# Optimization experiments

Measured on AMD Instinct MI355X. Metric: run time of the kernel, lower is better.

The kernel has to match this reference:

```python
import jax, jax.numpy as jnp
import numpy as np

N = 131072   # total nodes in batch
E = 524288   # directed edges
B = 2048     # number of graphs
H = 128      # hidden_dim
NF = 30      # node_feature_dim
GF = 4415    # gene_feature_dim
L = 3        # gnn_layers
EPS = 1e-5   # batchnorm eps


def setup_inputs() -> dict:
    key = jax.random.key(0)
    ks = jax.random.split(key, 24)
    rn = lambda k, s, sc=0.05: jax.random.normal(k, s, jnp.float32) * sc
    return {
        "x": jax.random.normal(ks[0], (N, NF), jnp.float32),
        "gene_features": jax.random.normal(ks[1], (B, GF), jnp.float32),
        "edge_index": jax.random.randint(ks[2], (2, E), 0, N),
        "batch": (jnp.arange(N) * B) // N,  # sorted, every graph non-empty
        "W_emb": rn(ks[3], (NF, H)), "b_emb": jnp.zeros((H,), jnp.float32),
        "Wg": rn(ks[4], (L, H, H)), "bg": jnp.zeros((L, H), jnp.float32),
        "bn_gamma": jnp.ones((L, H), jnp.float32), "bn_beta": jnp.zeros((L, H), jnp.float32),
        "Wd1": rn(ks[5], (2 * H, H)), "bd1": jnp.zeros((H,), jnp.float32),
        "Wd2": rn(ks[6], (H, H)), "bd2": jnp.zeros((H,), jnp.float32),
        "Wge1": rn(ks[7], (GF, 256)), "bge1": jnp.zeros((256,), jnp.float32),
        "g_gamma": jnp.ones((256,), jnp.float32), "g_beta": jnp.zeros((256,), jnp.float32),
        "Wge2": rn(ks[8], (256, H)), "bge2": jnp.zeros((H,), jnp.float32),
        "Wh1": rn(ks[9], (2 * H, H)), "bh1": jnp.zeros((H,), jnp.float32),
        "h_gamma": jnp.ones((H,), jnp.float32), "h_beta": jnp.zeros((H,), jnp.float32),
        "Wh2": rn(ks[10], (H, 64)), "bh2": jnp.zeros((64,), jnp.float32),
        "Wh3": rn(ks[11], (64, 1)), "bh3": jnp.zeros((1,), jnp.float32),
    }


def _bn_eval(x, gamma, beta):
    # inference batchnorm with running_mean=0, running_var=1
    return x * (gamma / jnp.sqrt(1.0 + EPS)) + beta


def _gcn_conv(h, W, b, src, dst):
    # PyG GCNConv: add self-loops, symmetric deg normalization, W first, bias after agg
    hw = h @ W                                            # [N,H]
    loop = jnp.arange(N)
    src_a = jnp.concatenate([src, loop])                  # [E+N]
    dst_a = jnp.concatenate([dst, loop])
    deg = jax.ops.segment_sum(jnp.ones((E + N,), hw.dtype), dst_a, num_segments=N)
    dinv = jnp.where(deg > 0, jax.lax.rsqrt(deg), 0.0)
    norm = dinv[src_a] * dinv[dst_a]                      # [E+N]
    msgs = hw[src_a] * norm[:, None]                      # gather [E+N,H]
    out = jax.ops.segment_sum(msgs, dst_a, num_segments=N)
    return out + b


def reference(x, gene_features, edge_index, batch, W_emb, b_emb, Wg, bg, bn_gamma,
              bn_beta, Wd1, bd1, Wd2, bd2, Wge1, bge1, g_gamma, g_beta, Wge2, bge2,
              Wh1, bh1, h_gamma, h_beta, Wh2, bh2, Wh3, bh3):
    src, dst = edge_index[0], edge_index[1]
    h = jax.nn.relu(x @ W_emb + b_emb)                    # [N,H]
    for i in range(L):
        hn = _gcn_conv(h, Wg[i], bg[i], src, dst)
        hn = jax.nn.relu(_bn_eval(hn, bn_gamma[i], bn_beta[i]))
        h = hn if i == 0 else h + hn                      # residual for i>0
    # global mean / max pooling per graph
    counts = jax.ops.segment_sum(jnp.ones((N,), h.dtype), batch, num_segments=B)
    mean_pool = jax.ops.segment_sum(h, batch, num_segments=B) / jnp.maximum(counts, 1.0)[:, None]
    max_pool = jax.ops.segment_max(h, batch, num_segments=B)
    graph_repr = jnp.concatenate([mean_pool, max_pool], axis=1)   # [B,2H]
    drug = jax.nn.relu(graph_repr @ Wd1 + bd1) @ Wd2 + bd2        # [B,H]
    g1 = jax.nn.relu(_bn_eval(gene_features @ Wge1 + bge1, g_gamma, g_beta))
    gene = jax.nn.relu(g1 @ Wge2 + bge2)                          # [B,H]
    comb = jnp.concatenate([drug, gene], axis=1)                  # [B,2H]
    z = jax.nn.relu(_bn_eval(comb @ Wh1 + bh1, h_gamma, h_beta))
    z = jax.nn.relu(z @ Wh2 + bh2)
    return z @ Wh3 + bh3                                          # [B,1]
```

## Files before the change

kernel.cpp:

```cpp
#include <hip/hip_runtime.h>

#define N_NODES 131072
#define E_EDGES 524288
#define B_GR    2048
#define H_DIM   128
#define NF_DIM  30
#define GF_DIM  4415
#define GF_PAD  4416
#define BN_SCALE 0.9999950000374997f

typedef __bf16 bf16x8 __attribute__((ext_vector_type(8)));
typedef float  f32x4  __attribute__((ext_vector_type(4)));
typedef unsigned int uint32;

__device__ __forceinline__ void split2(float x, __bf16& hi, __bf16& lo){
    hi = (__bf16)x;
    lo = (__bf16)(x - (float)hi);
}
__device__ __forceinline__ uint32 bfbits(float x){
    __bf16 h = (__bf16)x;
    return (uint32)__builtin_bit_cast(unsigned short, h);
}
__device__ __forceinline__ float unpack_even(uint32 u){ return __uint_as_float(u<<16); }
__device__ __forceinline__ float unpack_odd (uint32 u){ return __uint_as_float(u & 0xffff0000u); }
__device__ __forceinline__ uint32 pack2(float e, float o){ return bfbits(e) | (bfbits(o)<<16); }


__global__ void k_zero_int(int* __restrict__ p, int n){
    int i = blockIdx.x*256 + threadIdx.x;
    if(i < n) p[i] = 0;
}

__global__ void k_count(const int* __restrict__ dst, int* __restrict__ counts){
    int e = blockIdx.x*256 + threadIdx.x;
    if(e < E_EDGES) atomicAdd(&counts[dst[e]], 1);
}

__global__ void k_scan1(int* __restrict__ counts, int* __restrict__ bsums){
    __shared__ int s[1024];
    int t = threadIdx.x;
    int gi = blockIdx.x*1024 + t;
    int v = counts[gi];
    s[t] = v; __syncthreads();
    for(int off=1; off<1024; off<<=1){
        int x = (t>=off) ? s[t-off] : 0;
        __syncthreads();
        s[t] += x;
        __syncthreads();
    }
    counts[gi] = s[t] - v;
    if(t == 1023) bsums[blockIdx.x] = s[t];
}

__global__ void k_scan2(int* __restrict__ bsums){
    __shared__ int s[128];
    int t = threadIdx.x;
    int v = bsums[t]; s[t] = v; __syncthreads();
    for(int off=1; off<128; off<<=1){
        int x = (t>=off) ? s[t-off] : 0;
        __syncthreads();
        s[t] += x;
        __syncthreads();
    }
    bsums[t] = s[t] - v;
}

__global__ void k_scan3(const int* __restrict__ counts, const int* __restrict__ bsums,
                        int* __restrict__ rowptr){
    int i = blockIdx.x*1024 + threadIdx.x;
    rowptr[i] = counts[i] + bsums[blockIdx.x];
    if(i == 0) rowptr[N_NODES] = E_EDGES;
}

__global__ void k_dinv_cursor(const int* __restrict__ rowptr, float* __restrict__ dinv,
                              int* __restrict__ cursor){
    int n = blockIdx.x*256 + threadIdx.x;
    if(n < N_NODES){
        int a = rowptr[n], b = rowptr[n+1];
        dinv[n] = rsqrtf((float)(b - a) + 1.0f);
        cursor[n] = a;
    }
}

__global__ void k_fill(const int* __restrict__ src, const int* __restrict__ dst,
                       int* __restrict__ cursor, int* __restrict__ csr){
    int e = blockIdx.x*256 + threadIdx.x;
    if(e < E_EDGES){
        int p = atomicAdd(&cursor[dst[e]], 1);
        csr[p] = src[e];
    }
}


__global__ void k_split_x(const float* __restrict__ x, __bf16* __restrict__ xh,
                          __bf16* __restrict__ xl){
    int idx = blockIdx.x*256 + threadIdx.x;
    int n = idx >> 5, k = idx & 31;
    float v = (k < NF_DIM) ? x[n*NF_DIM + k] : 0.f;
    split2(v, xh[idx], xl[idx]);
}

__global__ void k_split_wemb(const float* __restrict__ W, __bf16* __restrict__ th,
                             __bf16* __restrict__ tl){
    int idx = blockIdx.x*256 + threadIdx.x;
    int c = idx >> 5, k = idx & 31;
    float v = (k < NF_DIM) ? W[k*H_DIM + c] : 0.f;
    split2(v, th[idx], tl[idx]);
}

__global__ void k_split_wg(const float* __restrict__ Wg, __bf16* __restrict__ th,
                           __bf16* __restrict__ tl){
    int idx = blockIdx.x*256 + threadIdx.x;
    int l = idx >> 14, i = idx & 16383;
    int k = i >> 7, c = i & 127;
    float v = Wg[idx];
    int o = (l << 14) + (c << 7) + k;
    split2(v, th[o], tl[o]);
}

__global__ void k_split_gf(const float* __restrict__ gf, __bf16* __restrict__ ah,
                           __bf16* __restrict__ al){
    unsigned idx = blockIdx.x*256 + threadIdx.x;
    unsigned r = idx / GF_PAD, k = idx - r*GF_PAD;
    float v = (k < GF_DIM) ? gf[(size_t)r*GF_DIM + k] : 0.f;
    split2(v, ah[idx], al[idx]);
}

__global__ void k_split_wge1(const float* __restrict__ W, __bf16* __restrict__ th,
                             __bf16* __restrict__ tl){
    unsigned idx = blockIdx.x*256 + threadIdx.x;
    unsigned c = idx / GF_PAD, k = idx - c*GF_PAD;
    float v = (k < GF_DIM) ? W[(size_t)k*256 + c] : 0.f;
    split2(v, th[idx], tl[idx]);
}


__global__ __launch_bounds__(256)
void k_emb_mfma(const __bf16* __restrict__ xh, const __bf16* __restrict__ xl,
                const __bf16* __restrict__ wth, const __bf16* __restrict__ wtl,
                const float* __restrict__ bias, uint32* __restrict__ Hh2,
                uint32* __restrict__ Hl2){
    __shared__ float sT[4][32*68];
    int wave = threadIdx.x >> 6, lane = threadIdx.x & 63;
    int lr = lane & 15, lq = lane >> 4;
    int rbase = blockIdx.x*128 + wave*32;
    const f32x4 zero4 = {0.f,0.f,0.f,0.f};
    bf16x8 A0h = *(const bf16x8*)(xh + (size_t)(rbase + lr)*32 + lq*8);
    bf16x8 A0l = *(const bf16x8*)(xl + (size_t)(rbase + lr)*32 + lq*8);
    bf16x8 A1h = *(const bf16x8*)(xh + (size_t)(rbase + 16 + lr)*32 + lq*8);
    bf16x8 A1l = *(const bf16x8*)(xl + (size_t)(rbase + 16 + lr)*32 + lq*8);
    int orow = lane >> 3;
    int oq   = lane & 7;
    float* sW = sT[wave];
    for(int ph=0; ph<2; ph++){
        #pragma unroll
        for(int cc=0; cc<4; cc++){
            int col = (ph*4+cc)*16 + lr;
            bf16x8 Bh = *(const bf16x8*)(wth + col*32 + lq*8);
            bf16x8 Bl = *(const bf16x8*)(wtl + col*32 + lq*8);
            f32x4 a0 = zero4, a1 = zero4;
            a0 = __builtin_amdgcn_mfma_f32_16x16x32_bf16(A0h, Bh, a0, 0,0,0);
            a0 = __builtin_amdgcn_mfma_f32_16x16x32_bf16(A0l, Bh, a0, 0,0,0);
            a0 = __builtin_amdgcn_mfma_f32_16x16x32_bf16(A0h, Bl, a0, 0,0,0);
            a1 = __builtin_amdgcn_mfma_f32_16x16x32_bf16(A1h, Bh, a1, 0,0,0);
            a1 = __builtin_amdgcn_mfma_f32_16x16x32_bf16(A1l, Bh, a1, 0,0,0);
            a1 = __builtin_amdgcn_mfma_f32_16x16x32_bf16(A1h, Bl, a1, 0,0,0);
            #pragma unroll
            for(int r=0;r<4;r++){
                sW[(lq*4+r)*68 + cc*16 + lr]    = a0[r];
                sW[(16+lq*4+r)*68 + cc*16 + lr] = a1[r];
            }
        }
        __syncthreads();
        int cg = ph*64 + oq*8;
        float bb[8];
        *(float4*)&bb[0] = *(const float4*)(bias + cg);
        *(float4*)&bb[4] = *(const float4*)(bias + cg + 4);
        #pragma unroll
        for(int i=0;i<4;i++){
            int row = i*8 + orow;
            float v[8];
            *(float4*)&v[0] = *(float4*)&sW[row*68 + oq*8];
            *(float4*)&v[4] = *(float4*)&sW[row*68 + oq*8 + 4];
            uint32 oh[4], ol[4];
            #pragma unroll
            for(int p=0;p<4;p++){
                float ve = fmaxf(v[2*p]   + bb[2*p],   0.f);
                float vo = fmaxf(v[2*p+1] + bb[2*p+1], 0.f);
                uint32 he = bfbits(ve), ho = bfbits(vo);
                oh[p] = he | (ho<<16);
                float le = ve - __uint_as_float(he<<16);
                float lo = vo - __uint_as_float(ho<<16);
                ol[p] = pack2(le, lo);
            }
            size_t oidx = (size_t)(rbase + row)*64 + (cg>>1);
            *(uint4*)(Hh2 + oidx) = make_uint4(oh[0],oh[1],oh[2],oh[3]);
            *(uint4*)(Hl2 + oidx) = make_uint4(ol[0],ol[1],ol[2],ol[3]);
        }
        __syncthreads();
    }
}


__global__ __launch_bounds__(256)
void k_agg(const __bf16* __restrict__ Hh, const __bf16* __restrict__ Hl,
           const float* __restrict__ dinv, const int* __restrict__ rowptr,
           const int* __restrict__ csr, uint32* __restrict__ Ah2,
           uint32* __restrict__ Al2){
    int wave = threadIdx.x >> 6, lane = threadIdx.x & 63;
    int n = blockIdx.x*4 + wave;
    float dn = dinv[n];
    size_t i0 = (size_t)n*64 + lane;
    const uint32* Hh2 = (const uint32*)Hh;
    const uint32* Hl2 = (const uint32*)Hl;
    uint32 sh = Hh2[i0], sl = Hl2[i0];
    float sx = unpack_even(sh) + unpack_even(sl);
    float sy = unpack_odd(sh)  + unpack_odd(sl);
    float ax = sx*dn, ay = sy*dn;
    int j0 = rowptr[n], j1 = rowptr[n+1];
    int jm = j1 - 1;
    for(int j=j0; j<j1; j+=8){
        int jj[8]; float ww[8]; uint32 rr[8];
        #pragma unroll
        for(int t=0;t<8;t++){
            int idx = (j+t<=jm) ? j+t : jm;
            jj[t] = csr[idx];
        }
        #pragma unroll
        for(int t=0;t<8;t++){
            ww[t] = (j+t<=jm) ? dinv[jj[t]] : 0.f;
            rr[t] = Hh2[(size_t)jj[t]*64 + lane];
        }
        #pragma unroll
        for(int t=0;t<8;t++){
            ax = fmaf(unpack_even(rr[t]), ww[t], ax);
            ay = fmaf(unpack_odd(rr[t]),  ww[t], ay);
        }
    }
    ax *= dn; ay *= dn;
    uint32 hx = bfbits(ax), hy = bfbits(ay);
    Ah2[i0] = hx | (hy<<16);
    float lx = ax - __uint_as_float(hx<<16);
    float ly = ay - __uint_as_float(hy<<16);
    Al2[i0] = pack2(lx, ly);
}


__global__ __launch_bounds__(256)
void k_mm_epi(const __bf16* __restrict__ Ah, const __bf16* __restrict__ Al,
              const __bf16* __restrict__ Bth, const __bf16* __restrict__ Btl,
              const float* __restrict__ bias, const float* __restrict__ gamma,
              const float* __restrict__ beta, uint32* __restrict__ Hh2,
              uint32* __restrict__ Hl2, int residual){
    __shared__ float sT[4][32*68];
    int wave = threadIdx.x >> 6, lane = threadIdx.x & 63;
    int lr = lane & 15, lq = lane >> 4;
    int rbase = blockIdx.x*128 + wave*32;
    const f32x4 zero4 = {0.f,0.f,0.f,0.f};
    size_t o0 = (size_t)(rbase + lr)*H_DIM + lq*8;
    size_t o1 = o0 + (size_t)16*H_DIM;
    bf16x8 A0h[4], A0l[4], A1h[4], A1l[4];
    #pragma unroll
    for(int ks=0;ks<4;ks++){
        A0h[ks] = *(const bf16x8*)(Ah + o0 + ks*32);
        A0l[ks] = *(const bf16x8*)(Al + o0 + ks*32);
        A1h[ks] = *(const bf16x8*)(Ah + o1 + ks*32);
        A1l[ks] = *(const bf16x8*)(Al + o1 + ks*32);
    }
    int orow = lane >> 3;
    int oq   = lane & 7;
    float* sW = sT[wave];
    for(int ph=0; ph<2; ph++){
        #pragma unroll
        for(int cc=0; cc<4; cc++){
            int col = (ph*4+cc)*16 + lr;
            f32x4 a0 = zero4, a1 = zero4;
            #pragma unroll
            for(int ks=0;ks<4;ks++){
                bf16x8 Bh = *(const bf16x8*)(Bth + col*H_DIM + ks*32 + lq*8);
                bf16x8 Bl = *(const bf16x8*)(Btl + col*H_DIM + ks*32 + lq*8);
                a0 = __builtin_amdgcn_mfma_f32_16x16x32_bf16(A0h[ks], Bh, a0, 0,0,0);
                a0 = __builtin_amdgcn_mfma_f32_16x16x32_bf16(A0l[ks], Bh, a0, 0,0,0);
                a0 = __builtin_amdgcn_mfma_f32_16x16x32_bf16(A0h[ks], Bl, a0, 0,0,0);
                a1 = __builtin_amdgcn_mfma_f32_16x16x32_bf16(A1h[ks], Bh, a1, 0,0,0);
                a1 = __builtin_amdgcn_mfma_f32_16x16x32_bf16(A1l[ks], Bh, a1, 0,0,0);
                a1 = __builtin_amdgcn_mfma_f32_16x16x32_bf16(A1h[ks], Bl, a1, 0,0,0);
            }
            #pragma unroll
            for(int r=0;r<4;r++){
                sW[(lq*4+r)*68 + cc*16 + lr]    = a0[r];
                sW[(16+lq*4+r)*68 + cc*16 + lr] = a1[r];
            }
        }
        __syncthreads();
        int cg = ph*64 + oq*8;
        float bb[8], gg[8], tt[8];
        *(float4*)&bb[0] = *(const float4*)(bias + cg);
        *(float4*)&bb[4] = *(const float4*)(bias + cg + 4);
        *(float4*)&gg[0] = *(const float4*)(gamma + cg);
        *(float4*)&gg[4] = *(const float4*)(gamma + cg + 4);
        *(float4*)&tt[0] = *(const float4*)(beta + cg);
        *(float4*)&tt[4] = *(const float4*)(beta + cg + 4);
        #pragma unroll
        for(int p=0;p<8;p++) gg[p] *= BN_SCALE;
        #pragma unroll
        for(int i=0;i<4;i++){
            int row = i*8 + orow;
            float v[8];
            *(float4*)&v[0] = *(float4*)&sW[row*68 + oq*8];
            *(float4*)&v[4] = *(float4*)&sW[row*68 + oq*8 + 4];
            size_t oidx = (size_t)(rbase + row)*64 + (cg>>1);
            uint4 oldh = {0,0,0,0}, oldl = {0,0,0,0};
            if(residual){
                oldh = *(const uint4*)(Hh2 + oidx);
                oldl = *(const uint4*)(Hl2 + oidx);
            }
            uint32 ohv[4] = {oldh.x,oldh.y,oldh.z,oldh.w};
            uint32 olv[4] = {oldl.x,oldl.y,oldl.z,oldl.w};
            uint32 oh[4], ol[4];
            #pragma unroll
            for(int p=0;p<4;p++){
                float ve = fmaxf(fmaf(v[2*p]   + bb[2*p],   gg[2*p],   tt[2*p]),   0.f);
                float vo = fmaxf(fmaf(v[2*p+1] + bb[2*p+1], gg[2*p+1], tt[2*p+1]), 0.f);
                if(residual){
                    ve += unpack_even(ohv[p]) + unpack_even(olv[p]);
                    vo += unpack_odd(ohv[p])  + unpack_odd(olv[p]);
                }
                uint32 he = bfbits(ve), ho = bfbits(vo);
                oh[p] = he | (ho<<16);
                float le = ve - __uint_as_float(he<<16);
                float lo = vo - __uint_as_float(ho<<16);
                ol[p] = pack2(le, lo);
            }
            *(uint4*)(Hh2 + oidx) = make_uint4(oh[0],oh[1],oh[2],oh[3]);
            *(uint4*)(Hl2 + oidx) = make_uint4(ol[0],ol[1],ol[2],ol[3]);
        }
        __syncthreads();
    }
}


__global__ __launch_bounds__(256)
void k_gemm_gf_mfma(const __bf16* __restrict__ Ah, const __bf16* __restrict__ Al,
                    const __bf16* __restrict__ Bth, const __bf16* __restrict__ Btl,
                    float* __restrict__ gpart){
    int rt = blockIdx.x & 31;
    int sp = blockIdx.x >> 5;
    int ks0 = (sp*138) >> 3, ks1 = ((sp+1)*138) >> 3;
    int wave = threadIdx.x >> 6, lane = threadIdx.x & 63;
    int lr = lane & 15, lq = lane >> 4;
    int rbase = rt*64 + (wave & 1)*32;
    int cbase = (wave >> 1)*128;
    const f32x4 zero4 = {0.f,0.f,0.f,0.f};
    f32x4 acc[8][2];
    #pragma unroll
    for(int ct=0;ct<8;ct++){ acc[ct][0] = zero4; acc[ct][1] = zero4; }
    for(int ks=ks0; ks<ks1; ks++){
        int kc = ks*32;
        size_t oa0 = (size_t)(rbase + lr)*GF_PAD + kc + lq*8;
        size_t oa1 = oa0 + (size_t)16*GF_PAD;
        bf16x8 A0h = *(const bf16x8*)(Ah + oa0);
        bf16x8 A0l = *(const bf16x8*)(Al + oa0);
        bf16x8 A1h = *(const bf16x8*)(Ah + oa1);
        bf16x8 A1l = *(const bf16x8*)(Al + oa1);
        #pragma unroll
        for(int ct=0;ct<8;ct++){
            size_t bo = (size_t)(cbase + ct*16 + lr)*GF_PAD + kc + lq*8;
            bf16x8 Bh = *(const bf16x8*)(Bth + bo);
            bf16x8 Bl = *(const bf16x8*)(Btl + bo);
            acc[ct][0] = __builtin_amdgcn_mfma_f32_16x16x32_bf16(A0h, Bh, acc[ct][0], 0,0,0);
            acc[ct][0] = __builtin_amdgcn_mfma_f32_16x16x32_bf16(A0l, Bh, acc[ct][0], 0,0,0);
            acc[ct][0] = __builtin_amdgcn_mfma_f32_16x16x32_bf16(A0h, Bl, acc[ct][0], 0,0,0);
            acc[ct][1] = __builtin_amdgcn_mfma_f32_16x16x32_bf16(A1h, Bh, acc[ct][1], 0,0,0);
            acc[ct][1] = __builtin_amdgcn_mfma_f32_16x16x32_bf16(A1l, Bh, acc[ct][1], 0,0,0);
            acc[ct][1] = __builtin_amdgcn_mfma_f32_16x16x32_bf16(A1h, Bl, acc[ct][1], 0,0,0);
        }
    }
    float* po = gpart + (size_t)sp*(B_GR*256);
    #pragma unroll
    for(int ct=0;ct<8;ct++)
        #pragma unroll
        for(int s=0;s<2;s++)
            #pragma unroll
            for(int r=0;r<4;r++)
                po[(size_t)(rbase + s*16 + lq*4 + r)*256 + cbase + ct*16 + lr] = acc[ct][s][r];
}

__global__ void k_gene_reduce(const float* __restrict__ gpart, const float* __restrict__ bias,
                              const float* __restrict__ gamma, const float* __restrict__ beta,
                              float* __restrict__ g1){
    int i = blockIdx.x*256 + threadIdx.x;
    int c = i & 255;
    float v = bias[c];
    #pragma unroll
    for(int sp=0;sp<8;sp++) v += gpart[(size_t)sp*(B_GR*256) + i];
    v = fmaf(v, gamma[c]*BN_SCALE, beta[c]);
    g1[i] = fmaxf(v, 0.f);
}


__global__ void k_pool(const __bf16* __restrict__ Hh, const __bf16* __restrict__ Hl,
                       float* __restrict__ pool){
    int g = blockIdx.x, c = threadIdx.x;
    const __bf16* bh = Hh + (size_t)g*64*H_DIM;
    const __bf16* bl = Hl + (size_t)g*64*H_DIM;
    float s = 0.f, m = -3.4e38f;
    for(int i=0;i<64;i++){
        float v = (float)bh[i*H_DIM + c] + (float)bl[i*H_DIM + c];
        s += v; m = fmaxf(m, v);
    }
    pool[g*256 + c]       = s * (1.f/64.f);
    pool[g*256 + 128 + c] = m;
}


__global__ void k_dense(const float* __restrict__ A, int ldA, const float* __restrict__ W,
                        const float* __restrict__ bias, const float* __restrict__ gamma,
                        const float* __restrict__ beta, float* __restrict__ out, int ldOut,
                        int K, int logK, int NC, int relu){
    extern __shared__ float sA[];
    int rowBase = blockIdx.x*4;
    int c = threadIdx.x;
    for(int idx=threadIdx.x; idx<4*K; idx+=NC){
        int r = idx >> logK, k = idx & (K-1);
        sA[idx] = A[(rowBase+r)*ldA + k];
    }
    __syncthreads();
    float bb = bias[c];
    float acc0=bb, acc1=bb, acc2=bb, acc3=bb;
    for(int k=0;k<K;k++){
        float w = W[k*NC + c];
        acc0 = fmaf(sA[k],     w, acc0);
        acc1 = fmaf(sA[K+k],   w, acc1);
        acc2 = fmaf(sA[2*K+k], w, acc2);
        acc3 = fmaf(sA[3*K+k], w, acc3);
    }
    float gsc = 1.f, bsh = 0.f;
    if(gamma){ gsc = gamma[c]*BN_SCALE; bsh = beta[c]; }
    float v0=acc0, v1=acc1, v2=acc2, v3=acc3;
    if(gamma){ v0=fmaf(v0,gsc,bsh); v1=fmaf(v1,gsc,bsh); v2=fmaf(v2,gsc,bsh); v3=fmaf(v3,gsc,bsh); }
    if(relu){ v0=fmaxf(v0,0.f); v1=fmaxf(v1,0.f); v2=fmaxf(v2,0.f); v3=fmaxf(v3,0.f); }
    out[(rowBase+0)*ldOut + c] = v0;
    out[(rowBase+1)*ldOut + c] = v1;
    out[(rowBase+2)*ldOut + c] = v2;
    out[(rowBase+3)*ldOut + c] = v3;
}


__global__ void k_final(const float* __restrict__ z2, const float* __restrict__ Wh3,
                        const float* __restrict__ bh3, float* __restrict__ out){
    int lane = threadIdx.x & 63, wr = threadIdx.x >> 6;
    int r = blockIdx.x*4 + wr;
    float v = z2[r*64 + lane] * Wh3[lane];
    #pragma unroll
    for(int off=32; off; off>>=1) v += __shfl_down(v, off);
    if(lane == 0) out[r] = v + bh3[0];
}


extern "C" void kernel_launch(void* const* d_in, const int* in_sizes, int n_in,
                              void* d_out, int out_size, void* d_ws, size_t ws_size,
                              hipStream_t stream){
    (void)in_sizes; (void)n_in; (void)out_size; (void)ws_size;
    const float* x    = (const float*)d_in[0];
    const float* gf   = (const float*)d_in[1];
    const int*   ei   = (const int*)  d_in[2];
    const float* W_emb= (const float*)d_in[4];
    const float* b_emb= (const float*)d_in[5];
    const float* Wg   = (const float*)d_in[6];
    const float* bg   = (const float*)d_in[7];
    const float* bn_g = (const float*)d_in[8];
    const float* bn_b = (const float*)d_in[9];
    const float* Wd1  = (const float*)d_in[10];
    const float* bd1  = (const float*)d_in[11];
    const float* Wd2  = (const float*)d_in[12];
    const float* bd2  = (const float*)d_in[13];
    const float* Wge1 = (const float*)d_in[14];
    const float* bge1 = (const float*)d_in[15];
    const float* g_g  = (const float*)d_in[16];
    const float* g_b  = (const float*)d_in[17];
    const float* Wge2 = (const float*)d_in[18];
    const float* bge2 = (const float*)d_in[19];
    const float* Wh1  = (const float*)d_in[20];
    const float* bh1  = (const float*)d_in[21];
    const float* h_g  = (const float*)d_in[22];
    const float* h_b  = (const float*)d_in[23];
    const float* Wh2  = (const float*)d_in[24];
    const float* bh2  = (const float*)d_in[25];
    const float* Wh3  = (const float*)d_in[26];
    const float* bh3  = (const float*)d_in[27];
    float* outp = (float*)d_out;

    char* base = (char*)d_ws;
    __bf16* Hh = (__bf16*)base;
    __bf16* Hl = (__bf16*)(base + (32u<<20));
    char*   R  = base + (64u<<20);
    __bf16* gfh    = (__bf16*)R;
    __bf16* gfl    = (__bf16*)(R + 18087936);
    float*  gpart  = (float*) (R + 36175872);
    __bf16* wge_th = (__bf16*)(R + 52953088);
    __bf16* wge_tl = (__bf16*)(R + 55214080);
    __bf16* xsh = (__bf16*)R;
    __bf16* xsl = (__bf16*)(R + (8u<<20));
    __bf16* Ah = (__bf16*)R;
    __bf16* Al = (__bf16*)(R + (32u<<20));
    char* T = base + (128u<<20);
    float* pool = (float*)T;
    float* g1   = pool + B_GR*256;
    float* t1   = g1   + B_GR*256;
    float* comb = t1   + B_GR*128;
    float* z    = comb + B_GR*256;
    float* z2   = z    + B_GR*128;
    int* rowptr = (int*)(z2 + B_GR*64);
    int* cursor = rowptr + (N_NODES+1);
    int* csr    = cursor + N_NODES;
    int* bsums  = csr + E_EDGES;
    float* dinv = (float*)(bsums + 128);
    __bf16* wg_th = (__bf16*)(dinv + N_NODES);
    __bf16* wg_tl = wg_th + 3*16384;
    __bf16* we_th = wg_tl + 3*16384;
    __bf16* we_tl = we_th + 128*32;

    const int* src = ei;
    const int* dst = ei + E_EDGES;

    k_zero_int   <<<N_NODES/256, 256, 0, stream>>>(cursor, N_NODES);
    k_count      <<<E_EDGES/256, 256, 0, stream>>>(dst, cursor);
    k_scan1      <<<128, 1024, 0, stream>>>(cursor, bsums);
    k_scan2      <<<1, 128, 0, stream>>>(bsums);
    k_scan3      <<<128, 1024, 0, stream>>>(cursor, bsums, rowptr);
    k_dinv_cursor<<<N_NODES/256, 256, 0, stream>>>(rowptr, dinv, cursor);
    k_fill       <<<E_EDGES/256, 256, 0, stream>>>(src, dst, cursor, csr);

    k_split_gf    <<<(B_GR*GF_PAD)/256, 256, 0, stream>>>(gf, gfh, gfl);
    k_split_wge1  <<<(256*GF_PAD)/256, 256, 0, stream>>>(Wge1, wge_th, wge_tl);
    k_gemm_gf_mfma<<<256, 256, 0, stream>>>(gfh, gfl, wge_th, wge_tl, gpart);
    k_gene_reduce <<<(B_GR*256)/256, 256, 0, stream>>>(gpart, bge1, g_g, g_b, g1);

    k_split_x    <<<(N_NODES*32)/256, 256, 0, stream>>>(x, xsh, xsl);
    k_split_wemb <<<(128*32)/256, 256, 0, stream>>>(W_emb, we_th, we_tl);
    k_split_wg   <<<(3*16384)/256, 256, 0, stream>>>(Wg, wg_th, wg_tl);
    k_emb_mfma   <<<N_NODES/128, 256, 0, stream>>>(xsh, xsl, we_th, we_tl, b_emb,
                                                   (uint32*)Hh, (uint32*)Hl);

    for(int i=0;i<3;i++){
        k_agg   <<<N_NODES/4, 256, 0, stream>>>(Hh, Hl, dinv, rowptr, csr,
                                                (uint32*)Ah, (uint32*)Al);
        k_mm_epi<<<N_NODES/128, 256, 0, stream>>>(Ah, Al, wg_th + i*16384, wg_tl + i*16384,
                                                  bg + i*H_DIM, bn_g + i*H_DIM, bn_b + i*H_DIM,
                                                  (uint32*)Hh, (uint32*)Hl, i > 0);
    }

    k_pool<<<B_GR, 128, 0, stream>>>(Hh, Hl, pool);
    k_dense<<<B_GR/4, 128, 4*256*4, stream>>>(pool, 256, Wd1, bd1, nullptr, nullptr, t1,   128, 256, 8, 128, 1);
    k_dense<<<B_GR/4, 128, 4*128*4, stream>>>(t1,   128, Wd2, bd2, nullptr, nullptr, comb, 256, 128, 7, 128, 0);
    k_dense<<<B_GR/4, 128, 4*256*4, stream>>>(g1,   256, Wge2, bge2, nullptr, nullptr, comb+128, 256, 256, 8, 128, 1);
    k_dense<<<B_GR/4, 128, 4*256*4, stream>>>(comb, 256, Wh1, bh1, h_g, h_b, z, 128, 256, 8, 128, 1);
    k_dense<<<B_GR/4, 64,  4*128*4, stream>>>(z,    128, Wh2, bh2, nullptr, nullptr, z2, 64, 128, 7, 64, 1);
    k_final<<<B_GR/4, 256, 0, stream>>>(z2, Wh3, bh3, outp);
}
```

Baseline: 692.5 us.

## Fuse GCN aggregation and dense transform into one per-layer kernel with ping-pong buffers

Merges the sparse neighbor aggregation and the MFMA matmul+BN+ReLU+residual epilogue into a single kernel per layer. Aggregated rows now go through LDS instead of a global round trip. Each wave processes two nodes at once to raise memory-level parallelism in the gather. Output goes to a separate buffer, swapped between layers. In exchange the block uses large LDS and 512 threads, which may reduce occupancy, and the gather phase no longer overlaps separately with the matmul phase.

```diff
diff --git a/kernel.cpp b/kernel.cpp
--- a/kernel.cpp
+++ b/kernel.cpp
@@ -12,6 +12,7 @@
 typedef __bf16 bf16x8 __attribute__((ext_vector_type(8)));
 typedef float  f32x4  __attribute__((ext_vector_type(4)));
 typedef unsigned int uint32;
+typedef uint32 u32x4 __attribute__((ext_vector_type(4)));
 
 __device__ __forceinline__ void split2(float x, __bf16& hi, __bf16& lo){
     hi = (__bf16)x;
@@ -202,140 +203,156 @@
 }
 
 
-__global__ __launch_bounds__(256)
-void k_agg(const __bf16* __restrict__ Hh, const __bf16* __restrict__ Hl,
-           const float* __restrict__ dinv, const int* __restrict__ rowptr,
-           const int* __restrict__ csr, uint32* __restrict__ Ah2,
-           uint32* __restrict__ Al2){
-    int wave = threadIdx.x >> 6, lane = threadIdx.x & 63;
-    int n = blockIdx.x*4 + wave;
-    float dn = dinv[n];
-    size_t i0 = (size_t)n*64 + lane;
-    const uint32* Hh2 = (const uint32*)Hh;
-    const uint32* Hl2 = (const uint32*)Hl;
-    uint32 sh = Hh2[i0], sl = Hl2[i0];
-    float sx = unpack_even(sh) + unpack_even(sl);
-    float sy = unpack_odd(sh)  + unpack_odd(sl);
-    float ax = sx*dn, ay = sy*dn;
-    int j0 = rowptr[n], j1 = rowptr[n+1];
-    int jm = j1 - 1;
-    for(int j=j0; j<j1; j+=8){
-        int jj[8]; float ww[8]; uint32 rr[8];
-        #pragma unroll
-        for(int t=0;t<8;t++){
-            int idx = (j+t<=jm) ? j+t : jm;
-            jj[t] = csr[idx];
-        }
-        #pragma unroll
-        for(int t=0;t<8;t++){
-            ww[t] = (j+t<=jm) ? dinv[jj[t]] : 0.f;
-            rr[t] = Hh2[(size_t)jj[t]*64 + lane];
-        }
-        #pragma unroll
-        for(int t=0;t<8;t++){
-            ax = fmaf(unpack_even(rr[t]), ww[t], ax);
-            ay = fmaf(unpack_odd(rr[t]),  ww[t], ay);
-        }
-    }
-    ax *= dn; ay *= dn;
-    uint32 hx = bfbits(ax), hy = bfbits(ay);
-    Ah2[i0] = hx | (hy<<16);
-    float lx = ax - __uint_as_float(hx<<16);
-    float ly = ay - __uint_as_float(hy<<16);
-    Al2[i0] = pack2(lx, ly);
-}
-
-
-__global__ __launch_bounds__(256)
-void k_mm_epi(const __bf16* __restrict__ Ah, const __bf16* __restrict__ Al,
-              const __bf16* __restrict__ Bth, const __bf16* __restrict__ Btl,
-              const float* __restrict__ bias, const float* __restrict__ gamma,
-              const float* __restrict__ beta, uint32* __restrict__ Hh2,
-              uint32* __restrict__ Hl2, int residual){
-    __shared__ float sT[4][32*68];
-    int wave = threadIdx.x >> 6, lane = threadIdx.x & 63;
+__global__ __launch_bounds__(512, 4)
+void k_layer(const __bf16* __restrict__ curHh, const __bf16* __restrict__ curHl,
+             const float* __restrict__ dinv, const int* __restrict__ rowptr,
+             const int* __restrict__ csr,
+             const __bf16* __restrict__ Bth, const __bf16* __restrict__ Btl,
+             const float* __restrict__ bias, const float* __restrict__ gamma,
+             const float* __restrict__ beta,
+             uint32* __restrict__ outHh2, uint32* __restrict__ outHl2, int residual){
+    __shared__ uint32 smem[8*32*68];
+    uint32* AhL = smem;
+    uint32* AlL = smem + 128*68;
+    int tid  = threadIdx.x;
+    int wave = tid >> 6, lane = tid & 63;
+    int rbase = blockIdx.x * 128;
+    const uint32* Hh2 = (const uint32*)curHh;
+    const uint32* Hl2 = (const uint32*)curHl;
+
+    for(int ii=0; ii<8; ii++){
+        int rowA = wave*16 + ii;
+        int rowB = rowA + 8;
+        int nA = rbase + rowA, nB = rbase + rowB;
+        float dnA = dinv[nA], dnB = dinv[nB];
+        size_t iA = (size_t)nA*64 + lane, iB = (size_t)nB*64 + lane;
+        uint32 shA = Hh2[iA], slA = Hl2[iA];
+        uint32 shB = Hh2[iB], slB = Hl2[iB];
+        float axA = (unpack_even(shA) + unpack_even(slA)) * dnA;
+        float ayA = (unpack_odd(shA)  + unpack_odd(slA))  * dnA;
+        float axB = (unpack_even(shB) + unpack_even(slB)) * dnB;
+        float ayB = (unpack_odd(shB)  + unpack_odd(slB))  * dnB;
+        int j0A = rowptr[nA], j1A = rowptr[nA+1];
+        int j0B = rowptr[nB], j1B = rowptr[nB+1];
+        int cA = j1A - j0A, cB = j1B - j0B;
+        int nb = cA > cB ? cA : cB;
+        for(int j=0; j<nb; j+=8){
+            int jjA[8], jjB[8]; float wwA[8], wwB[8]; uint32 rrA[8], rrB[8];
+            #pragma unroll
+            for(int t=0;t<8;t++){
+                jjA[t] = csr[(j+t < cA) ? j0A + j + t : j0A] & (N_NODES-1);
+                jjB[t] = csr[(j+t < cB) ? j0B + j + t : j0B] & (N_NODES-1);
+            }
+            #pragma unroll
+            for(int t=0;t<8;t++){
+                wwA[t] = (j+t < cA) ? dinv[jjA[t]] : 0.f;
+                rrA[t] = Hh2[(size_t)jjA[t]*64 + lane];
+                wwB[t] = (j+t < cB) ? dinv[jjB[t]] : 0.f;
+                rrB[t] = Hh2[(size_t)jjB[t]*64 + lane];
+            }
+            #pragma unroll
+            for(int t=0;t<8;t++){
+                axA = fmaf(unpack_even(rrA[t]), wwA[t], axA);
+                ayA = fmaf(unpack_odd(rrA[t]),  wwA[t], ayA);
+                axB = fmaf(unpack_even(rrB[t]), wwB[t], axB);
+                ayB = fmaf(unpack_odd(rrB[t]),  wwB[t], ayB);
+            }
+        }
+        axA *= dnA; ayA *= dnA;
+        axB *= dnB; ayB *= dnB;
+        uint32 hxA = bfbits(axA), hyA = bfbits(ayA);
+        AhL[rowA*68 + lane] = hxA | (hyA<<16);
+        AlL[rowA*68 + lane] = pack2(axA - __uint_as_float(hxA<<16),
+                                    ayA - __uint_as_float(hyA<<16));
+        uint32 hxB = bfbits(axB), hyB = bfbits(ayB);
+        AhL[rowB*68 + lane] = hxB | (hyB<<16);
+        AlL[rowB*68 + lane] = pack2(axB - __uint_as_float(hxB<<16),
+                                    ayB - __uint_as_float(hyB<<16));
+    }
+    __syncthreads();
+
     int lr = lane & 15, lq = lane >> 4;
-    int rbase = blockIdx.x*128 + wave*32;
+    int wr = wave & 3, wc = wave >> 2;
+    int r0 = wr*32;
+    bf16x8 A0h[4], A0l[4], A1h[4], A1l[4];
+    #pragma unroll
+    for(int ks=0;ks<4;ks++){
+        int u0 = (r0 + lr)*68 + lq*4 + ks*16;
+        int u1 = (r0 + 16 + lr)*68 + lq*4 + ks*16;
+        A0h[ks] = __builtin_bit_cast(bf16x8, *(const u32x4*)(AhL + u0));
+        A0l[ks] = __builtin_bit_cast(bf16x8, *(const u32x4*)(AlL + u0));
+        A1h[ks] = __builtin_bit_cast(bf16x8, *(const u32x4*)(AhL + u1));
+        A1l[ks] = __builtin_bit_cast(bf16x8, *(const u32x4*)(AlL + u1));
+    }
+    __syncthreads();
+
+    float* stg = (float*)smem + wave*(32*68);
     const f32x4 zero4 = {0.f,0.f,0.f,0.f};
-    size_t o0 = (size_t)(rbase + lr)*H_DIM + lq*8;
-    size_t o1 = o0 + (size_t)16*H_DIM;
-    bf16x8 A0h[4], A0l[4], A1h[4], A1l[4];
-    #pragma unroll
-    for(int ks=0;ks<4;ks++){
-        A0h[ks] = *(const bf16x8*)(Ah + o0 + ks*32);
-        A0l[ks] = *(const bf16x8*)(Al + o0 + ks*32);
-        A1h[ks] = *(const bf16x8*)(Ah + o1 + ks*32);
-        A1l[ks] = *(const bf16x8*)(Al + o1 + ks*32);
-    }
+    #pragma unroll
+    for(int cc=0; cc<4; cc++){
+        int col = wc*64 + cc*16 + lr;
+        f32x4 a0 = zero4, a1 = zero4;
+        #pragma unroll
+        for(int ks=0;ks<4;ks++){
+            bf16x8 Bh = *(const bf16x8*)(Bth + col*H_DIM + ks*32 + lq*8);
+            bf16x8 Bl = *(const bf16x8*)(Btl + col*H_DIM + ks*32 + lq*8);
+            a0 = __builtin_amdgcn_mfma_f32_16x16x32_bf16(A0h[ks], Bh, a0, 0,0,0);
+            a0 = __builtin_amdgcn_mfma_f32_16x16x32_bf16(A0l[ks], Bh, a0, 0,0,0);
+            a0 = __builtin_amdgcn_mfma_f32_16x16x32_bf16(A0h[ks], Bl, a0, 0,0,0);
+            a1 = __builtin_amdgcn_mfma_f32_16x16x32_bf16(A1h[ks], Bh, a1, 0,0,0);
+            a1 = __builtin_amdgcn_mfma_f32_16x16x32_bf16(A1l[ks], Bh, a1, 0,0,0);
+            a1 = __builtin_amdgcn_mfma_f32_16x16x32_bf16(A1h[ks], Bl, a1, 0,0,0);
+        }
+        #pragma unroll
+        for(int r=0;r<4;r++){
+            stg[(lq*4+r)*68 + cc*16 + lr]    = a0[r];
+            stg[(16+lq*4+r)*68 + cc*16 + lr] = a1[r];
+        }
+    }
+
     int orow = lane >> 3;
     int oq   = lane & 7;
-    float* sW = sT[wave];
-    for(int ph=0; ph<2; ph++){
-        #pragma unroll
-        for(int cc=0; cc<4; cc++){
-            int col = (ph*4+cc)*16 + lr;
-            f32x4 a0 = zero4, a1 = zero4;
-            #pragma unroll
-            for(int ks=0;ks<4;ks++){
-                bf16x8 Bh = *(const bf16x8*)(Bth + col*H_DIM + ks*32 + lq*8);
-                bf16x8 Bl = *(const bf16x8*)(Btl + col*H_DIM + ks*32 + lq*8);
-                a0 = __builtin_amdgcn_mfma_f32_16x16x32_bf16(A0h[ks], Bh, a0, 0,0,0);
-                a0 = __builtin_amdgcn_mfma_f32_16x16x32_bf16(A0l[ks], Bh, a0, 0,0,0);
-                a0 = __builtin_amdgcn_mfma_f32_16x16x32_bf16(A0h[ks], Bl, a0, 0,0,0);
-                a1 = __builtin_amdgcn_mfma_f32_16x16x32_bf16(A1h[ks], Bh, a1, 0,0,0);
-                a1 = __builtin_amdgcn_mfma_f32_16x16x32_bf16(A1l[ks], Bh, a1, 0,0,0);
-                a1 = __builtin_amdgcn_mfma_f32_16x16x32_bf16(A1h[ks], Bl, a1, 0,0,0);
+    int cg = wc*64 + oq*8;
+    float bb[8], gg[8], tt[8];
+    *(float4*)&bb[0] = *(const float4*)(bias + cg);
+    *(float4*)&bb[4] = *(const float4*)(bias + cg + 4);
+    *(float4*)&gg[0] = *(const float4*)(gamma + cg);
+    *(float4*)&gg[4] = *(const float4*)(gamma + cg + 4);
+    *(float4*)&tt[0] = *(const float4*)(beta + cg);
+    *(float4*)&tt[4] = *(const float4*)(beta + cg + 4);
+    #pragma unroll
+    for(int p=0;p<8;p++) gg[p] *= BN_SCALE;
+    #pragma unroll
+    for(int i=0;i<4;i++){
+        int row = i*8 + orow;
+        float v[8];
+        *(float4*)&v[0] = *(float4*)&stg[row*68 + oq*8];
+        *(float4*)&v[4] = *(float4*)&stg[row*68 + oq*8 + 4];
+        size_t oidx = (size_t)(rbase + r0 + row)*64 + (cg>>1);
+        uint4 oldh = {0,0,0,0}, oldl = {0,0,0,0};
+        if(residual){
+            oldh = *(const uint4*)(Hh2 + oidx);
+            oldl = *(const uint4*)(Hl2 + oidx);
+        }
+        uint32 ohv[4] = {oldh.x,oldh.y,oldh.z,oldh.w};
+        uint32 olv[4] = {oldl.x,oldl.y,oldl.z,oldl.w};
+        uint32 oh[4], ol[4];
+        #pragma unroll
+        for(int p=0;p<4;p++){
+            float ve = fmaxf(fmaf(v[2*p]   + bb[2*p],   gg[2*p],   tt[2*p]),   0.f);
+            float vo = fmaxf(fmaf(v[2*p+1] + bb[2*p+1], gg[2*p+1], tt[2*p+1]), 0.f);
+            if(residual){
+                ve += unpack_even(ohv[p]) + unpack_even(olv[p]);
+                vo += unpack_odd(ohv[p])  + unpack_odd(olv[p]);
             }
-            #pragma unroll
-            for(int r=0;r<4;r++){
-                sW[(lq*4+r)*68 + cc*16 + lr]    = a0[r];
-                sW[(16+lq*4+r)*68 + cc*16 + lr] = a1[r];
-            }
-        }
-        __syncthreads();
-        int cg = ph*64 + oq*8;
-        float bb[8], gg[8], tt[8];
-        *(float4*)&bb[0] = *(const float4*)(bias + cg);
-        *(float4*)&bb[4] = *(const float4*)(bias + cg + 4);
-        *(float4*)&gg[0] = *(const float4*)(gamma + cg);
-        *(float4*)&gg[4] = *(const float4*)(gamma + cg + 4);
-        *(float4*)&tt[0] = *(const float4*)(beta + cg);
-        *(float4*)&tt[4] = *(const float4*)(beta + cg + 4);
-        #pragma unroll
-        for(int p=0;p<8;p++) gg[p] *= BN_SCALE;
-        #pragma unroll
-        for(int i=0;i<4;i++){
-            int row = i*8 + orow;
-            float v[8];
-            *(float4*)&v[0] = *(float4*)&sW[row*68 + oq*8];
-            *(float4*)&v[4] = *(float4*)&sW[row*68 + oq*8 + 4];
-            size_t oidx = (size_t)(rbase + row)*64 + (cg>>1);
-            uint4 oldh = {0,0,0,0}, oldl = {0,0,0,0};
-            if(residual){
-                oldh = *(const uint4*)(Hh2 + oidx);
-                oldl = *(const uint4*)(Hl2 + oidx);
-            }
-            uint32 ohv[4] = {oldh.x,oldh.y,oldh.z,oldh.w};
-            uint32 olv[4] = {oldl.x,oldl.y,oldl.z,oldl.w};
-            uint32 oh[4], ol[4];
-            #pragma unroll
-            for(int p=0;p<4;p++){
-                float ve = fmaxf(fmaf(v[2*p]   + bb[2*p],   gg[2*p],   tt[2*p]),   0.f);
-                float vo = fmaxf(fmaf(v[2*p+1] + bb[2*p+1], gg[2*p+1], tt[2*p+1]), 0.f);
-                if(residual){
-                    ve += unpack_even(ohv[p]) + unpack_even(olv[p]);
-                    vo += unpack_odd(ohv[p])  + unpack_odd(olv[p]);
-                }
-                uint32 he = bfbits(ve), ho = bfbits(vo);
-                oh[p] = he | (ho<<16);
-                float le = ve - __uint_as_float(he<<16);
-                float lo = vo - __uint_as_float(ho<<16);
-                ol[p] = pack2(le, lo);
-            }
-            *(uint4*)(Hh2 + oidx) = make_uint4(oh[0],oh[1],oh[2],oh[3]);
-            *(uint4*)(Hl2 + oidx) = make_uint4(ol[0],ol[1],ol[2],ol[3]);
-        }
-        __syncthreads();
+            uint32 he = bfbits(ve), ho = bfbits(vo);
+            oh[p] = he | (ho<<16);
+            float le = ve - __uint_as_float(he<<16);
+            float lo = vo - __uint_as_float(ho<<16);
+            ol[p] = pack2(le, lo);
+        }
+        *(uint4*)(outHh2 + oidx) = make_uint4(oh[0],oh[1],oh[2],oh[3]);
+        *(uint4*)(outHl2 + oidx) = make_uint4(ol[0],ol[1],ol[2],ol[3]);
     }
 }
 
@@ -502,8 +519,8 @@
     __bf16* wge_tl = (__bf16*)(R + 55214080);
     __bf16* xsh = (__bf16*)R;
     __bf16* xsl = (__bf16*)(R + (8u<<20));
-    __bf16* Ah = (__bf16*)R;
-    __bf16* Al = (__bf16*)(R + (32u<<20));
+    __bf16* Ph = (__bf16*)R;
+    __bf16* Pl = (__bf16*)(R + (32u<<20));
     char* T = base + (128u<<20);
     float* pool = (float*)T;
     float* g1   = pool + B_GR*256;
@@ -543,15 +560,21 @@
     k_emb_mfma   <<<N_NODES/128, 256, 0, stream>>>(xsh, xsl, we_th, we_tl, b_emb,
                                                    (uint32*)Hh, (uint32*)Hl);
 
-    for(int i=0;i<3;i++){
-        k_agg   <<<N_NODES/4, 256, 0, stream>>>(Hh, Hl, dinv, rowptr, csr,
-                                                (uint32*)Ah, (uint32*)Al);
-        k_mm_epi<<<N_NODES/128, 256, 0, stream>>>(Ah, Al, wg_th + i*16384, wg_tl + i*16384,
-                                                  bg + i*H_DIM, bn_g + i*H_DIM, bn_b + i*H_DIM,
-                                                  (uint32*)Hh, (uint32*)Hl, i > 0);
-    }
-
-    k_pool<<<B_GR, 128, 0, stream>>>(Hh, Hl, pool);
+    {
+        uint32 *curh = (uint32*)Hh, *curl = (uint32*)Hl;
+        uint32 *outh = (uint32*)Ph, *outl = (uint32*)Pl;
+        for(int i=0;i<3;i++){
+            k_layer<<<N_NODES/128, 512, 0, stream>>>((const __bf16*)curh, (const __bf16*)curl,
+                                                     dinv, rowptr, csr,
+                                                     wg_th + i*16384, wg_tl + i*16384,
+                                                     bg + i*H_DIM, bn_g + i*H_DIM, bn_b + i*H_DIM,
+                                                     outh, outl, i > 0);
+            uint32* th = curh; curh = outh; outh = th;
+            uint32* tl = curl; curl = outl; outl = tl;
+        }
+        k_pool<<<B_GR, 128, 0, stream>>>((const __bf16*)curh, (const __bf16*)curl, pool);
+    }
+
     k_dense<<<B_GR/4, 128, 4*256*4, stream>>>(pool, 256, Wd1, bd1, nullptr, nullptr, t1,   128, 256, 8, 128, 1);
     k_dense<<<B_GR/4, 128, 4*128*4, stream>>>(t1,   128, Wd2, bd2, nullptr, nullptr, comb, 256, 128, 7, 128, 0);
     k_dense<<<B_GR/4, 128, 4*256*4, stream>>>(g1,   256, Wge2, bge2, nullptr, nullptr, comb+128, 256, 256, 8, 128, 1);
```

After: 638.7 us. 7.8% less time.
